# Kernel tuning notes

Measured on AMD Instinct MI355X. Metric: run time of the kernel, lower is better.

Reference implementation:

```python
import jax, jax.numpy as jnp
import numpy as np

N_NODES = 100000
N_EDGES = 1600000
D_FEAT = 128
NUM_UNITS = 128


def setup_inputs() -> dict:
    key = jax.random.key(0)
    k1, k2, k3, k4, k5 = jax.random.split(key, 5)
    H = jax.random.normal(k1, (N_NODES, D_FEAT), dtype=jnp.float32)
    edge_vals = jax.random.uniform(k2, (N_EDGES,), dtype=jnp.float32)
    W = jax.random.normal(k3, (D_FEAT, NUM_UNITS), dtype=jnp.float32) / np.sqrt(D_FEAT)
    b = jnp.zeros((NUM_UNITS,), dtype=jnp.float32)
    edge_src = jax.random.randint(k4, (N_EDGES,), 0, N_NODES, dtype=jnp.int32)
    edge_dst = jax.random.randint(k5, (N_EDGES,), 0, N_NODES, dtype=jnp.int32)
    return {"H": H, "edge_vals": edge_vals, "W": W, "b": b,
            "edge_src": edge_src, "edge_dst": edge_dst}


def reference(H, edge_vals, W, b, edge_src, edge_dst):
    # SpMM: AH[i] = sum_{e: src[e]==i} val[e] * H[dst[e]]
    gathered = edge_vals[:, None] * H[edge_dst]            # [E, F]
    AH = jax.ops.segment_sum(gathered, edge_src, num_segments=N_NODES)  # [N, F]
    # Dense projection + bias + relu (tf.layers.Dense with tf.nn.relu)
    return jax.nn.relu(AH @ W + b)
```

## Files before the change

### kernel.cpp

```cpp
#include <hip/hip_runtime.h>

#define N_NODES  100000
#define N_EDGES  1600000
#define D        128
#define NBUCK    3125
#define BCAP     768
#define OCAP     8192
#define FCHUNK   8192
#define FILL_BLOCKS ((N_EDGES + FCHUNK - 1) / FCHUNK)
#define NPACK    ((NBUCK + 1) / 2)

typedef __attribute__((ext_vector_type(8))) short bf16x8;
typedef __attribute__((ext_vector_type(4))) float f32x4;

__device__ __forceinline__ unsigned short f2bf(float x) {
    unsigned u = __float_as_uint(x);
    u += 0x7fffu + ((u >> 16) & 1u);
    return (unsigned short)(u >> 16);
}

__global__ __launch_bounds__(256) void init_kernel(
    const float* __restrict__ W, unsigned short* __restrict__ Wfrag,
    int* __restrict__ ccursor)
{
    int t = blockIdx.x * 256 + threadIdx.x;
    if (t <= NBUCK) ccursor[t] = 0;
    int k = t >> 7, n = t & 127;
    int c = n >> 4, cc = n & 15, ks = k >> 5, g = (k >> 3) & 3, j = k & 7;
    int lane = g * 16 + cc;
    Wfrag[(size_t)(((c * 4 + ks) * 64) + lane) * 8 + j] = f2bf(W[t]);
}

__global__ __launch_bounds__(256) void gemm_mfma(
    const float* __restrict__ H, const unsigned short* __restrict__ Wfrag,
    unsigned short* __restrict__ HWb)
{
    const int wid  = threadIdx.x >> 6;
    const int lane = threadIdx.x & 63;
    const int row16 = blockIdx.x * 64 + wid * 16;
    const int g = lane >> 4;

    int arow = row16 + (lane & 15);
    if (arow >= N_NODES) arow = N_NODES - 1;

    f32x4 acc[8];
#pragma unroll
    for (int c = 0; c < 8; ++c) acc[c] = (f32x4){0.f, 0.f, 0.f, 0.f};

#pragma unroll
    for (int ks = 0; ks < 4; ++ks) {
        const float* ap = H + (size_t)arow * D + ks * 32 + g * 8;
        float4 a0 = *reinterpret_cast<const float4*>(ap);
        float4 a1 = *reinterpret_cast<const float4*>(ap + 4);
        bf16x8 af;
        af[0] = (short)f2bf(a0.x); af[1] = (short)f2bf(a0.y);
        af[2] = (short)f2bf(a0.z); af[3] = (short)f2bf(a0.w);
        af[4] = (short)f2bf(a1.x); af[5] = (short)f2bf(a1.y);
        af[6] = (short)f2bf(a1.z); af[7] = (short)f2bf(a1.w);
#pragma unroll
        for (int c = 0; c < 8; ++c) {
            bf16x8 bf = *reinterpret_cast<const bf16x8*>(
                Wfrag + (size_t)((c * 4 + ks) * 64 + lane) * 8);
            acc[c] = __builtin_amdgcn_mfma_f32_16x16x32_bf16(af, bf, acc[c], 0, 0, 0);
        }
    }

#pragma unroll
    for (int c = 0; c < 8; ++c) {
#pragma unroll
        for (int r = 0; r < 4; ++r) {
            int orow = row16 + g * 4 + r;
            if (orow < N_NODES)
                HWb[(size_t)orow * D + c * 16 + (lane & 15)] = f2bf(acc[c][r]);
        }
    }
}

__global__ __launch_bounds__(256) void fill_bucket(
    const int* __restrict__ src, const int* __restrict__ dst,
    const float* __restrict__ vals, int* __restrict__ ccursor,
    int2* __restrict__ sedge_raw, int4* __restrict__ oflow,
    int* __restrict__ oflow_cnt)
{
    __shared__ unsigned lhistP[NPACK];
    __shared__ unsigned lbaseP[NPACK];
    const int t = threadIdx.x;

    for (int i = t; i < NPACK; i += 256) lhistP[i] = 0;
    __syncthreads();
    const int e0 = blockIdx.x * FCHUNK;
    const int e1 = min(e0 + FCHUNK, N_EDGES);
    for (int e = e0 + t; e < e1; e += 256) {
        int b = src[e] >> 5;
        atomicAdd(&lhistP[b >> 1], 1u << ((b & 1) << 4));
    }
    __syncthreads();
    for (int i = t; i < NPACK; i += 256) {
        unsigned p = lhistP[i];
        unsigned c0 = p & 0xffffu, c1 = p >> 16;
        unsigned b0 = c0 ? (unsigned)atomicAdd(&ccursor[2 * i], (int)c0) : 0u;
        unsigned b1 = c1 ? (unsigned)atomicAdd(&ccursor[2 * i + 1], (int)c1) : 0u;
        lbaseP[i] = (b0 & 0xffffu) | (b1 << 16);
        lhistP[i] = 0;
    }
    __syncthreads();
    for (int e = e0 + t; e < e1; e += 256) {
        int s = src[e];
        int b = s >> 5;
        unsigned sh = (unsigned)(b & 1) << 4;
        unsigned old = atomicAdd(&lhistP[b >> 1], 1u << sh);
        int pos = (int)((lbaseP[b >> 1] >> sh) & 0xffffu) +
                  (int)((old >> sh) & 0xffffu);
        if (pos < BCAP) {
            int2 p;
            p.x = dst[e] | ((s & 31) << 17);
            p.y = __float_as_int(vals[e]);
            sedge_raw[(size_t)b * BCAP + pos] = p;
        } else {
            int oc = atomicAdd(oflow_cnt, 1);
            if (oc < OCAP) oflow[oc] = make_int4(s, dst[e], __float_as_int(vals[e]), 0);
        }
    }
}

__global__ __launch_bounds__(256) void sort_gather(
    const unsigned short* __restrict__ HWb, const int2* __restrict__ sedge_raw,
    const int* __restrict__ ccursor, const int4* __restrict__ oflow,
    const int* __restrict__ oflow_cnt, const float* __restrict__ bias,
    float* __restrict__ out)
{
    __shared__ int2 eLds[BCAP];
    __shared__ int h[32];
    __shared__ int ex[32];
    __shared__ int cur[32];
    const int bkt = blockIdx.x;
    const int t = threadIdx.x;
    const size_t base = (size_t)bkt * BCAP;
    const int cnt = min(ccursor[bkt], BCAP);

    if (t < 32) { h[t] = 0; }
    __syncthreads();

    int2 myE[3]; int myR[3];
#pragma unroll
    for (int q = 0; q < 3; ++q) {
        int j = t + q * 256;
        myR[q] = -1;
        if (j < cnt) {
            myE[q] = sedge_raw[base + j];
            myR[q] = (myE[q].x >> 17) & 31;
            atomicAdd(&h[myR[q]], 1);
        }
    }
    __syncthreads();
    if (t < 32) {
        int v = h[t];
        int x = v;
        for (int off = 1; off < 32; off <<= 1) {
            int y = __shfl_up(x, off);
            if (t >= off) x += y;
        }
        ex[t] = x - v;
        cur[t] = 0;
    }
    __syncthreads();
#pragma unroll
    for (int q = 0; q < 3; ++q) {
        if (myR[q] >= 0) {
            int pos = ex[myR[q]] + atomicAdd(&cur[myR[q]], 1);
            int2 e;
            e.x = myE[q].x & 0x1FFFF;
            e.y = myE[q].y;
            eLds[pos] = e;
        }
    }
    __syncthreads();

    const int wid = t >> 6, lane = t & 63;
    const int ovc = *oflow_cnt;
    const float2 bv = *reinterpret_cast<const float2*>(bias + lane * 2);
    for (int ln = wid; ln < 32; ln += 4) {
        int node = bkt * 32 + ln;
        const int j0 = ex[ln], j1 = ex[ln] + h[ln];
        float ax = 0.f, ay = 0.f, bx = 0.f, by = 0.f;
        float cx = 0.f, cy = 0.f, dx = 0.f, dy = 0.f;
        int j = j0;
        for (; j + 4 <= j1; j += 4) {
            int2 e0 = eLds[j],     e1 = eLds[j + 1];
            int2 e2 = eLds[j + 2], e3 = eLds[j + 3];
            unsigned u0 = *reinterpret_cast<const unsigned*>(HWb + (size_t)e0.x * D + lane * 2);
            unsigned u1 = *reinterpret_cast<const unsigned*>(HWb + (size_t)e1.x * D + lane * 2);
            unsigned u2 = *reinterpret_cast<const unsigned*>(HWb + (size_t)e2.x * D + lane * 2);
            unsigned u3 = *reinterpret_cast<const unsigned*>(HWb + (size_t)e3.x * D + lane * 2);
            float v0 = __int_as_float(e0.y), v1 = __int_as_float(e1.y);
            float v2 = __int_as_float(e2.y), v3 = __int_as_float(e3.y);
            ax += v0 * __uint_as_float(u0 << 16);
            ay += v0 * __uint_as_float(u0 & 0xffff0000u);
            bx += v1 * __uint_as_float(u1 << 16);
            by += v1 * __uint_as_float(u1 & 0xffff0000u);
            cx += v2 * __uint_as_float(u2 << 16);
            cy += v2 * __uint_as_float(u2 & 0xffff0000u);
            dx += v3 * __uint_as_float(u3 << 16);
            dy += v3 * __uint_as_float(u3 & 0xffff0000u);
        }
        for (; j < j1; ++j) {
            int2 e = eLds[j];
            unsigned u = *reinterpret_cast<const unsigned*>(HWb + (size_t)e.x * D + lane * 2);
            float v = __int_as_float(e.y);
            ax += v * __uint_as_float(u << 16);
            ay += v * __uint_as_float(u & 0xffff0000u);
        }
        for (int q = 0; q < ovc; ++q) {
            int4 e = oflow[q];
            if (e.x == node) {
                unsigned u = *reinterpret_cast<const unsigned*>(HWb + (size_t)e.y * D + lane * 2);
                float v = __int_as_float(e.z);
                ax += v * __uint_as_float(u << 16);
                ay += v * __uint_as_float(u & 0xffff0000u);
            }
        }
        float2 o;
        o.x = fmaxf((ax + bx) + (cx + dx) + bv.x, 0.f);
        o.y = fmaxf((ay + by) + (cy + dy) + bv.y, 0.f);
        *reinterpret_cast<float2*>(out + (size_t)node * D + lane * 2) = o;
    }
}

extern "C" void kernel_launch(void* const* d_in, const int* in_sizes, int n_in,
                              void* d_out, int out_size, void* d_ws, size_t ws_size,
                              hipStream_t stream) {
    const float* H    = (const float*)d_in[0];
    const float* vals = (const float*)d_in[1];
    const float* W    = (const float*)d_in[2];
    const float* b    = (const float*)d_in[3];
    const int*   src  = (const int*)d_in[4];
    const int*   dst  = (const int*)d_in[5];
    float* out = (float*)d_out;

    unsigned short* HWb   = (unsigned short*)d_ws;
    unsigned short* Wfrag = HWb + (size_t)N_NODES * D;
    int2* sedge_raw = (int2*)(Wfrag + 128 * 128);
    int*  ccursor   = (int*)(sedge_raw + (size_t)NBUCK * BCAP);
    int*  oflow_cnt = ccursor + NBUCK;
    int4* oflow     = (int4*)(oflow_cnt + 3);

    init_kernel<<<64, 256, 0, stream>>>(W, Wfrag, ccursor);
    gemm_mfma<<<(N_NODES + 63) / 64, 256, 0, stream>>>(H, Wfrag, HWb);
    fill_bucket<<<FILL_BLOCKS, 256, 0, stream>>>(src, dst, vals, ccursor,
                                                 sedge_raw, oflow, oflow_cnt);
    sort_gather<<<NBUCK, 256, 0, stream>>>(HWb, sedge_raw, ccursor, oflow,
                                           oflow_cnt, b, out);
}
```

Measured before the change: 140.8 us.

## Split bucket cursors into per-group sub-buckets to cut global atomic contention

Each source bucket now has 8 sub-buckets of capacity 128, selected by fill block index modulo 8, each with its own global cursor. This spreads the cross-block atomicAdd traffic on bucket cursors. The fill chunk drops to 2048 edges so there are more fill blocks, and the fill kernel now launches before the GEMM. The gather kernel prefix-sums the 8 sub-counts and maps each thread's slot to a sub-bucket with an unrolled search, which adds per-edge index work. The per-bucket LDS edge buffer grows to 1024 entries.

```diff
diff --git a/kernel.cpp b/kernel.cpp
--- a/kernel.cpp
+++ b/kernel.cpp
@@ -4,11 +4,13 @@
 #define N_EDGES  1600000
 #define D        128
 #define NBUCK    3125
-#define BCAP     768
+#define NGRP     8
+#define SUBCAP   128
 #define OCAP     8192
-#define FCHUNK   8192
+#define FCHUNK   2048
 #define FILL_BLOCKS ((N_EDGES + FCHUNK - 1) / FCHUNK)
 #define NPACK    ((NBUCK + 1) / 2)
+#define NCUR     (NBUCK * NGRP)
 
 typedef __attribute__((ext_vector_type(8))) short bf16x8;
 typedef __attribute__((ext_vector_type(4))) float f32x4;
@@ -24,11 +26,59 @@
     int* __restrict__ ccursor)
 {
     int t = blockIdx.x * 256 + threadIdx.x;
-    if (t <= NBUCK) ccursor[t] = 0;
+    for (int i = t; i <= NCUR; i += 64 * 256) ccursor[i] = 0;
     int k = t >> 7, n = t & 127;
     int c = n >> 4, cc = n & 15, ks = k >> 5, g = (k >> 3) & 3, j = k & 7;
     int lane = g * 16 + cc;
     Wfrag[(size_t)(((c * 4 + ks) * 64) + lane) * 8 + j] = f2bf(W[t]);
+}
+
+__global__ __launch_bounds__(256) void fill_bucket(
+    const int* __restrict__ src, const int* __restrict__ dst,
+    const float* __restrict__ vals, int* __restrict__ ccursor,
+    int2* __restrict__ sedge_raw, int4* __restrict__ oflow,
+    int* __restrict__ oflow_cnt)
+{
+    __shared__ unsigned lhistP[NPACK];
+    __shared__ unsigned lbaseP[NPACK];
+    const int t = threadIdx.x;
+    const int grp = blockIdx.x & (NGRP - 1);
+
+    for (int i = t; i < NPACK; i += 256) lhistP[i] = 0;
+    __syncthreads();
+    const int e0 = blockIdx.x * FCHUNK;
+    const int e1 = min(e0 + FCHUNK, N_EDGES);
+    for (int e = e0 + t; e < e1; e += 256) {
+        int bq = src[e] >> 5;
+        atomicAdd(&lhistP[bq >> 1], 1u << ((bq & 1) << 4));
+    }
+    __syncthreads();
+    for (int i = t; i < NPACK; i += 256) {
+        unsigned p = lhistP[i];
+        unsigned c0 = p & 0xffffu, c1 = p >> 16;
+        unsigned b0 = c0 ? (unsigned)atomicAdd(&ccursor[(2 * i) * NGRP + grp], (int)c0) : 0u;
+        unsigned b1 = c1 ? (unsigned)atomicAdd(&ccursor[(2 * i + 1) * NGRP + grp], (int)c1) : 0u;
+        lbaseP[i] = (b0 & 0xffffu) | (b1 << 16);
+        lhistP[i] = 0;
+    }
+    __syncthreads();
+    for (int e = e0 + t; e < e1; e += 256) {
+        int s = src[e];
+        int bq = s >> 5;
+        unsigned sh = (unsigned)(bq & 1) << 4;
+        unsigned old = atomicAdd(&lhistP[bq >> 1], 1u << sh);
+        int pos = (int)((lbaseP[bq >> 1] >> sh) & 0xffffu) +
+                  (int)((old >> sh) & 0xffffu);
+        if (pos < SUBCAP) {
+            int2 p;
+            p.x = dst[e] | ((s & 31) << 17);
+            p.y = __float_as_int(vals[e]);
+            sedge_raw[((size_t)bq * NGRP + grp) * SUBCAP + pos] = p;
+        } else {
+            int oc = atomicAdd(oflow_cnt, 1);
+            if (oc < OCAP) oflow[oc] = make_int4(s, dst[e], __float_as_int(vals[e]), 0);
+        }
+    }
 }
 
 __global__ __launch_bounds__(256) void gemm_mfma(
@@ -76,78 +126,45 @@
     }
 }
 
-__global__ __launch_bounds__(256) void fill_bucket(
-    const int* __restrict__ src, const int* __restrict__ dst,
-    const float* __restrict__ vals, int* __restrict__ ccursor,
-    int2* __restrict__ sedge_raw, int4* __restrict__ oflow,
-    int* __restrict__ oflow_cnt)
-{
-    __shared__ unsigned lhistP[NPACK];
-    __shared__ unsigned lbaseP[NPACK];
-    const int t = threadIdx.x;
-
-    for (int i = t; i < NPACK; i += 256) lhistP[i] = 0;
-    __syncthreads();
-    const int e0 = blockIdx.x * FCHUNK;
-    const int e1 = min(e0 + FCHUNK, N_EDGES);
-    for (int e = e0 + t; e < e1; e += 256) {
-        int b = src[e] >> 5;
-        atomicAdd(&lhistP[b >> 1], 1u << ((b & 1) << 4));
-    }
-    __syncthreads();
-    for (int i = t; i < NPACK; i += 256) {
-        unsigned p = lhistP[i];
-        unsigned c0 = p & 0xffffu, c1 = p >> 16;
-        unsigned b0 = c0 ? (unsigned)atomicAdd(&ccursor[2 * i], (int)c0) : 0u;
-        unsigned b1 = c1 ? (unsigned)atomicAdd(&ccursor[2 * i + 1], (int)c1) : 0u;
-        lbaseP[i] = (b0 & 0xffffu) | (b1 << 16);
-        lhistP[i] = 0;
-    }
-    __syncthreads();
-    for (int e = e0 + t; e < e1; e += 256) {
-        int s = src[e];
-        int b = s >> 5;
-        unsigned sh = (unsigned)(b & 1) << 4;
-        unsigned old = atomicAdd(&lhistP[b >> 1], 1u << sh);
-        int pos = (int)((lbaseP[b >> 1] >> sh) & 0xffffu) +
-                  (int)((old >> sh) & 0xffffu);
-        if (pos < BCAP) {
-            int2 p;
-            p.x = dst[e] | ((s & 31) << 17);
-            p.y = __float_as_int(vals[e]);
-            sedge_raw[(size_t)b * BCAP + pos] = p;
-        } else {
-            int oc = atomicAdd(oflow_cnt, 1);
-            if (oc < OCAP) oflow[oc] = make_int4(s, dst[e], __float_as_int(vals[e]), 0);
-        }
-    }
-}
-
 __global__ __launch_bounds__(256) void sort_gather(
     const unsigned short* __restrict__ HWb, const int2* __restrict__ sedge_raw,
     const int* __restrict__ ccursor, const int4* __restrict__ oflow,
     const int* __restrict__ oflow_cnt, const float* __restrict__ bias,
     float* __restrict__ out)
 {
-    __shared__ int2 eLds[BCAP];
+    __shared__ int2 eLds[NGRP * SUBCAP];
     __shared__ int h[32];
     __shared__ int ex[32];
     __shared__ int cur[32];
     const int bkt = blockIdx.x;
     const int t = threadIdx.x;
-    const size_t base = (size_t)bkt * BCAP;
-    const int cnt = min(ccursor[bkt], BCAP);
-
-    if (t < 32) { h[t] = 0; }
-    __syncthreads();
-
-    int2 myE[3]; int myR[3];
-#pragma unroll
-    for (int q = 0; q < 3; ++q) {
-        int j = t + q * 256;
+
+    int pfx[NGRP + 1];
+    pfx[0] = 0;
+#pragma unroll
+    for (int g = 0; g < NGRP; ++g) {
+        int c = ccursor[bkt * NGRP + g];
+        if (c > SUBCAP) c = SUBCAP;
+        pfx[g + 1] = pfx[g] + c;
+    }
+    const int tot = pfx[NGRP];
+
+    if (t < 32) h[t] = 0;
+    __syncthreads();
+
+    int2 myE[4]; int myR[4];
+#pragma unroll
+    for (int q = 0; q < 4; ++q) {
+        int jj = t + q * 256;
         myR[q] = -1;
-        if (j < cnt) {
-            myE[q] = sedge_raw[base + j];
+        if (jj < tot) {
+            int g = 0, j = jj;
+#pragma unroll
+            for (int gg = 0; gg < NGRP; ++gg) {
+                bool in = (jj >= pfx[gg]) && (jj < pfx[gg + 1]);
+                if (in) { g = gg; j = jj - pfx[gg]; }
+            }
+            myE[q] = sedge_raw[((size_t)bkt * NGRP + g) * SUBCAP + j];
             myR[q] = (myE[q].x >> 17) & 31;
             atomicAdd(&h[myR[q]], 1);
         }
@@ -165,7 +182,7 @@
     }
     __syncthreads();
 #pragma unroll
-    for (int q = 0; q < 3; ++q) {
+    for (int q = 0; q < 4; ++q) {
         if (myR[q] >= 0) {
             int pos = ex[myR[q]] + atomicAdd(&cur[myR[q]], 1);
             int2 e;
@@ -240,14 +257,14 @@
     unsigned short* HWb   = (unsigned short*)d_ws;
     unsigned short* Wfrag = HWb + (size_t)N_NODES * D;
     int2* sedge_raw = (int2*)(Wfrag + 128 * 128);
-    int*  ccursor   = (int*)(sedge_raw + (size_t)NBUCK * BCAP);
-    int*  oflow_cnt = ccursor + NBUCK;
+    int*  ccursor   = (int*)(sedge_raw + (size_t)NBUCK * NGRP * SUBCAP);
+    int*  oflow_cnt = ccursor + NCUR;
     int4* oflow     = (int4*)(oflow_cnt + 3);
 
     init_kernel<<<64, 256, 0, stream>>>(W, Wfrag, ccursor);
-    gemm_mfma<<<(N_NODES + 63) / 64, 256, 0, stream>>>(H, Wfrag, HWb);
     fill_bucket<<<FILL_BLOCKS, 256, 0, stream>>>(src, dst, vals, ccursor,
                                                  sedge_raw, oflow, oflow_cnt);
+    gemm_mfma<<<(N_NODES + 63) / 64, 256, 0, stream>>>(H, Wfrag, HWb);
     sort_gather<<<NBUCK, 256, 0, stream>>>(HWb, sedge_raw, ccursor, oflow,
                                            oflow_cnt, b, out);
 }
```

After: 178.4 us. +26.7%, slower.

## Coarsen edge buckets to 128 nodes and split each across four gather blocks

Applied to the files above, without the earlier changes.

The bucketing pass now scatters edges into 782 coarse buckets of 128 source nodes with plain int LDS histograms, replacing 3125 fine buckets packed as 16-bit pairs. Each sort_gather block reads the whole coarse bucket and keeps only the edges for its 32-node quarter. This cuts global atomics and cursor contention in the fill step, but each coarse bucket is read four times in the gather. The fill kernel is also launched before the GEMM. A new SUBCAP clamp can silently drop edges if a 32-node subgroup exceeds 768 edges.

```diff
diff --git a/kernel.cpp b/kernel.cpp
--- a/kernel.cpp
+++ b/kernel.cpp
@@ -3,12 +3,13 @@
 #define N_NODES  100000
 #define N_EDGES  1600000
 #define D        128
-#define NBUCK    3125
-#define BCAP     768
+#define CB       782
+#define CCAP     3072
+#define SUBCAP   768
 #define OCAP     8192
 #define FCHUNK   8192
 #define FILL_BLOCKS ((N_EDGES + FCHUNK - 1) / FCHUNK)
-#define NPACK    ((NBUCK + 1) / 2)
+#define NSG      3125
 
 typedef __attribute__((ext_vector_type(8))) short bf16x8;
 typedef __attribute__((ext_vector_type(4))) float f32x4;
@@ -24,11 +25,49 @@
     int* __restrict__ ccursor)
 {
     int t = blockIdx.x * 256 + threadIdx.x;
-    if (t <= NBUCK) ccursor[t] = 0;
+    if (t <= CB) ccursor[t] = 0;
     int k = t >> 7, n = t & 127;
     int c = n >> 4, cc = n & 15, ks = k >> 5, g = (k >> 3) & 3, j = k & 7;
     int lane = g * 16 + cc;
     Wfrag[(size_t)(((c * 4 + ks) * 64) + lane) * 8 + j] = f2bf(W[t]);
+}
+
+__global__ __launch_bounds__(256) void fill_bucket(
+    const int* __restrict__ src, const int* __restrict__ dst,
+    const float* __restrict__ vals, int* __restrict__ ccursor,
+    int2* __restrict__ sedge_raw, int4* __restrict__ oflow,
+    int* __restrict__ oflow_cnt)
+{
+    __shared__ int lhist[CB];
+    __shared__ int lbase[CB];
+    const int t = threadIdx.x;
+    for (int i = t; i < CB; i += 256) lhist[i] = 0;
+    __syncthreads();
+    const int e0 = blockIdx.x * FCHUNK;
+    const int e1 = min(e0 + FCHUNK, N_EDGES);
+    for (int e = e0 + t; e < e1; e += 256)
+        atomicAdd(&lhist[src[e] >> 7], 1);
+    __syncthreads();
+    for (int i = t; i < CB; i += 256) {
+        int c = lhist[i];
+        lbase[i] = c ? atomicAdd(&ccursor[i], c) : 0;
+        lhist[i] = 0;
+    }
+    __syncthreads();
+    for (int e = e0 + t; e < e1; e += 256) {
+        int s = src[e];
+        int bkt = s >> 7;
+        int pos = lbase[bkt] + atomicAdd(&lhist[bkt], 1);
+        if (pos < CCAP) {
+            int2 p;
+            p.x = dst[e] | ((s & 127) << 17);
+            p.y = __float_as_int(vals[e]);
+            sedge_raw[(size_t)bkt * CCAP + pos] = p;
+        } else {
+            int oc = atomicAdd(oflow_cnt, 1);
+            if (oc < OCAP) oflow[oc] = make_int4(s, dst[e], __float_as_int(vals[e]), 0);
+        }
+    }
 }
 
 __global__ __launch_bounds__(256) void gemm_mfma(
@@ -76,80 +115,37 @@
     }
 }
 
-__global__ __launch_bounds__(256) void fill_bucket(
-    const int* __restrict__ src, const int* __restrict__ dst,
-    const float* __restrict__ vals, int* __restrict__ ccursor,
-    int2* __restrict__ sedge_raw, int4* __restrict__ oflow,
-    int* __restrict__ oflow_cnt)
-{
-    __shared__ unsigned lhistP[NPACK];
-    __shared__ unsigned lbaseP[NPACK];
-    const int t = threadIdx.x;
-
-    for (int i = t; i < NPACK; i += 256) lhistP[i] = 0;
-    __syncthreads();
-    const int e0 = blockIdx.x * FCHUNK;
-    const int e1 = min(e0 + FCHUNK, N_EDGES);
-    for (int e = e0 + t; e < e1; e += 256) {
-        int b = src[e] >> 5;
-        atomicAdd(&lhistP[b >> 1], 1u << ((b & 1) << 4));
-    }
-    __syncthreads();
-    for (int i = t; i < NPACK; i += 256) {
-        unsigned p = lhistP[i];
-        unsigned c0 = p & 0xffffu, c1 = p >> 16;
-        unsigned b0 = c0 ? (unsigned)atomicAdd(&ccursor[2 * i], (int)c0) : 0u;
-        unsigned b1 = c1 ? (unsigned)atomicAdd(&ccursor[2 * i + 1], (int)c1) : 0u;
-        lbaseP[i] = (b0 & 0xffffu) | (b1 << 16);
-        lhistP[i] = 0;
-    }
-    __syncthreads();
-    for (int e = e0 + t; e < e1; e += 256) {
-        int s = src[e];
-        int b = s >> 5;
-        unsigned sh = (unsigned)(b & 1) << 4;
-        unsigned old = atomicAdd(&lhistP[b >> 1], 1u << sh);
-        int pos = (int)((lbaseP[b >> 1] >> sh) & 0xffffu) +
-                  (int)((old >> sh) & 0xffffu);
-        if (pos < BCAP) {
-            int2 p;
-            p.x = dst[e] | ((s & 31) << 17);
-            p.y = __float_as_int(vals[e]);
-            sedge_raw[(size_t)b * BCAP + pos] = p;
-        } else {
-            int oc = atomicAdd(oflow_cnt, 1);
-            if (oc < OCAP) oflow[oc] = make_int4(s, dst[e], __float_as_int(vals[e]), 0);
-        }
-    }
-}
-
 __global__ __launch_bounds__(256) void sort_gather(
     const unsigned short* __restrict__ HWb, const int2* __restrict__ sedge_raw,
     const int* __restrict__ ccursor, const int4* __restrict__ oflow,
     const int* __restrict__ oflow_cnt, const float* __restrict__ bias,
     float* __restrict__ out)
 {
-    __shared__ int2 eLds[BCAP];
+    __shared__ int2 eLds[SUBCAP];
     __shared__ int h[32];
     __shared__ int ex[32];
     __shared__ int cur[32];
-    const int bkt = blockIdx.x;
+    const int cb  = blockIdx.x >> 2;
+    const int sub = blockIdx.x & 3;
     const int t = threadIdx.x;
-    const size_t base = (size_t)bkt * BCAP;
-    const int cnt = min(ccursor[bkt], BCAP);
-
-    if (t < 32) { h[t] = 0; }
-    __syncthreads();
-
-    int2 myE[3]; int myR[3];
-#pragma unroll
-    for (int q = 0; q < 3; ++q) {
+    const size_t base = (size_t)cb * CCAP;
+    const int cnt = min(ccursor[cb], CCAP);
+
+    if (t < 32) h[t] = 0;
+    __syncthreads();
+
+    int2 myE[12]; int myR[12];
+#pragma unroll
+    for (int q = 0; q < 12; ++q) {
         int j = t + q * 256;
         myR[q] = -1;
         if (j < cnt) {
-            myE[q] = sedge_raw[base + j];
-            myR[q] = (myE[q].x >> 17) & 31;
-            atomicAdd(&h[myR[q]], 1);
+            int2 e = sedge_raw[base + j];
+            if (((e.x >> 22) & 3) == sub) {
+                myE[q] = e;
+                myR[q] = (e.x >> 17) & 31;
+                atomicAdd(&h[myR[q]], 1);
+            }
         }
     }
     __syncthreads();
@@ -165,13 +161,15 @@
     }
     __syncthreads();
 #pragma unroll
-    for (int q = 0; q < 3; ++q) {
+    for (int q = 0; q < 12; ++q) {
         if (myR[q] >= 0) {
             int pos = ex[myR[q]] + atomicAdd(&cur[myR[q]], 1);
-            int2 e;
-            e.x = myE[q].x & 0x1FFFF;
-            e.y = myE[q].y;
-            eLds[pos] = e;
+            if (pos < SUBCAP) {
+                int2 e;
+                e.x = myE[q].x & 0x1FFFF;
+                e.y = myE[q].y;
+                eLds[pos] = e;
+            }
         }
     }
     __syncthreads();
@@ -180,8 +178,9 @@
     const int ovc = *oflow_cnt;
     const float2 bv = *reinterpret_cast<const float2*>(bias + lane * 2);
     for (int ln = wid; ln < 32; ln += 4) {
-        int node = bkt * 32 + ln;
-        const int j0 = ex[ln], j1 = ex[ln] + h[ln];
+        int node = cb * 128 + sub * 32 + ln;
+        if (node >= N_NODES) break;
+        int j0 = ex[ln], j1 = min(ex[ln] + h[ln], SUBCAP);
         float ax = 0.f, ay = 0.f, bx = 0.f, by = 0.f;
         float cx = 0.f, cy = 0.f, dx = 0.f, dy = 0.f;
         int j = j0;
@@ -240,14 +239,14 @@
     unsigned short* HWb   = (unsigned short*)d_ws;
     unsigned short* Wfrag = HWb + (size_t)N_NODES * D;
     int2* sedge_raw = (int2*)(Wfrag + 128 * 128);
-    int*  ccursor   = (int*)(sedge_raw + (size_t)NBUCK * BCAP);
-    int*  oflow_cnt = ccursor + NBUCK;
+    int*  ccursor   = (int*)(sedge_raw + (size_t)CB * CCAP);
+    int*  oflow_cnt = ccursor + CB;
     int4* oflow     = (int4*)(oflow_cnt + 3);
 
     init_kernel<<<64, 256, 0, stream>>>(W, Wfrag, ccursor);
-    gemm_mfma<<<(N_NODES + 63) / 64, 256, 0, stream>>>(H, Wfrag, HWb);
     fill_bucket<<<FILL_BLOCKS, 256, 0, stream>>>(src, dst, vals, ccursor,
                                                  sedge_raw, oflow, oflow_cnt);
-    sort_gather<<<NBUCK, 256, 0, stream>>>(HWb, sedge_raw, ccursor, oflow,
-                                           oflow_cnt, b, out);
-}
+    gemm_mfma<<<(N_NODES + 63) / 64, 256, 0, stream>>>(H, Wfrag, HWb);
+    sort_gather<<<NSG, 256, 0, stream>>>(HWb, sedge_raw, ccursor, oflow,
+                                         oflow_cnt, b, out);
+}
```

Result: faster. 134.3 us (-4.6%).
